# Kernel optimization log

Measured on AMD Instinct MI355X. Metric: run time of the kernel, lower is better.

## Reference

```python
import jax, jax.numpy as jnp
import numpy as np

D_MODEL = 1024
N_HEADS = 16
D_K = D_MODEL // N_HEADS
D_FF = 4096
B, S = 2, 2048
LN_EPS = 1e-5
NEG_INF = -1e30  # finite stand-in for -inf; first (all-masked) row is overwritten by zeros anyway


def layer_norm(x, g, b):
    mu = jnp.mean(x, axis=-1, keepdims=True)
    var = jnp.mean(jnp.square(x - mu), axis=-1, keepdims=True)
    return (x - mu) * jax.lax.rsqrt(var + LN_EPS) * g + b


def setup_inputs() -> dict:
    key = jax.random.key(0)
    ks = jax.random.split(key, 16)
    sd = 0.02
    inp = {
        "query": jax.random.normal(ks[0], (B, S, D_MODEL), jnp.float32),
        "key": jax.random.normal(ks[1], (B, S, D_MODEL), jnp.float32),
        "values": jax.random.normal(ks[2], (B, S, D_MODEL), jnp.float32),
        "Wq": jax.random.normal(ks[3], (D_MODEL, D_MODEL), jnp.float32) * sd,
        "bq": jnp.zeros((D_MODEL,), jnp.float32),
        "Wk": jax.random.normal(ks[4], (D_MODEL, D_MODEL), jnp.float32) * sd,
        "bk": jnp.zeros((D_MODEL,), jnp.float32),
        "Wv": jax.random.normal(ks[5], (D_MODEL, D_MODEL), jnp.float32) * sd,
        "bv": jnp.zeros((D_MODEL,), jnp.float32),
        "Wo": jax.random.normal(ks[6], (D_MODEL, D_MODEL), jnp.float32) * sd,
        "bo": jnp.zeros((D_MODEL,), jnp.float32),
        "ln1_g": jnp.ones((D_MODEL,), jnp.float32),
        "ln1_b": jnp.zeros((D_MODEL,), jnp.float32),
        "W1": jax.random.normal(ks[7], (D_MODEL, D_FF), jnp.float32) * sd,
        "b1": jnp.zeros((D_FF,), jnp.float32),
        "W2": jax.random.normal(ks[8], (D_FF, D_MODEL), jnp.float32) * sd,
        "b2": jnp.zeros((D_MODEL,), jnp.float32),
        "ln2_g": jnp.ones((D_MODEL,), jnp.float32),
        "ln2_b": jnp.zeros((D_MODEL,), jnp.float32),
        "mask": 0,
    }
    return inp


def reference(query, key, values, Wq, bq, Wk, bk, Wv, bv, Wo, bo,
              ln1_g, ln1_b, W1, b1, W2, b2, ln2_g, ln2_b, mask):
    b, s, d = query.shape
    # projections -> [B, H, S, d_k]
    q = (query @ Wq + bq).reshape(b, s, N_HEADS, D_K).transpose(0, 2, 1, 3)
    k = (key @ Wk + bk).reshape(b, s, N_HEADS, D_K).transpose(0, 2, 1, 3)
    v = (values @ Wv + bv).reshape(b, s, N_HEADS, D_K).transpose(0, 2, 1, 3)
    # scores [B, H, S, S]
    scores = jnp.einsum("bhqd,bhkd->bhqk", q, k) / jnp.sqrt(jnp.float32(D_K))
    # torch: triu(ones, k=mask)==0 -> allowed iff j < i + mask
    i = jnp.arange(s)[:, None]
    j = jnp.arange(s)[None, :]
    allowed = j < (i + mask)
    scores = jnp.where(allowed, scores, NEG_INF)
    attn = jax.nn.softmax(scores, axis=-1)
    if mask == 0:
        # zero-pad trick: first query row (fully masked) is replaced by zeros
        attn = attn.at[:, :, 0, :].set(0.0)
    ctx = jnp.einsum("bhqk,bhkd->bhqd", attn, v)
    ctx = ctx.transpose(0, 2, 1, 3).reshape(b, s, d)
    attn_out = ctx @ Wo + bo
    x = layer_norm(query + attn_out, ln1_g, ln1_b)
    ffn = jax.nn.relu(x @ W1 + b1) @ W2 + b2
    out = layer_norm(x + ffn, ln2_g, ln2_b)
    return out
```

## Files before the change

kernel.cpp:

```cpp
#include <hip/hip_runtime.h>


typedef __attribute__((ext_vector_type(8))) __bf16 bf16x8;
typedef __attribute__((ext_vector_type(4))) float f32x4;
typedef __attribute__((ext_vector_type(8))) short s16x8;

struct alignas(8)  S4 { short x, y, z, w; };
struct alignas(16) F4 { float x, y, z, w; };

static __device__ __forceinline__ short f2bf(float f) {
  unsigned u = __float_as_uint(f);
  u += 0x7fff + ((u >> 16) & 1);
  return (short)(u >> 16);
}

static __device__ __forceinline__ short f2bf_fast(float f) {
  union { __bf16 h; short s; } u;
  u.h = (__bf16)f;
  return u.s;
}

#if __has_builtin(__builtin_amdgcn_exp2f)
#define EXP2F(x) __builtin_amdgcn_exp2f(x)
#else
#define EXP2F(x) exp2f(x)
#endif
#define SM_SCALE 0.18033688011112042f

static __device__ __forceinline__ void store_out(float* p, float v) { *p = v; }
static __device__ __forceinline__ void store_out(short* p, float v) { *p = f2bf(v); }

#define GLL16(g, l)                                                         \
  __builtin_amdgcn_global_load_lds(                                         \
      (__attribute__((address_space(1))) void*)(g),                         \
      (__attribute__((address_space(3))) void*)(l), 16, 0, 0)

__global__ __launch_bounds__(256) void cvt_bf16_kernel(
    const float* __restrict__ i0, const float* __restrict__ i1,
    const float* __restrict__ i2, short* __restrict__ o0,
    short* __restrict__ o1, short* __restrict__ o2) {
  int z = blockIdx.y;
  const float* in = z == 0 ? i0 : (z == 1 ? i1 : i2);
  short* out = z == 0 ? o0 : (z == 1 ? o1 : o2);
  int i = (blockIdx.x * 256 + threadIdx.x) * 4;
  F4 v = *(const F4*)(in + i);
  S4 o = { f2bf(v.x), f2bf(v.y), f2bf(v.z), f2bf(v.w) };
  *(S4*)(out + i) = o;
}

__global__ __launch_bounds__(256) void transpose_cvt_kernel(
    const float* __restrict__ Wq, const float* __restrict__ Wk,
    const float* __restrict__ Wv, const float* __restrict__ Wo,
    const float* __restrict__ W1, const float* __restrict__ W2,
    short* __restrict__ Wqt, short* __restrict__ Wkt,
    short* __restrict__ Wvt, short* __restrict__ Wot,
    short* __restrict__ W1t, short* __restrict__ W2t) {
  __shared__ float tile[64][65];
  int bid = blockIdx.x;
  const float* W; short* Wt; int K, N, kx, ny;
  if (bid < 1024) {
    int w = bid >> 8, t = bid & 255;
    W = w == 0 ? Wq : (w == 1 ? Wk : (w == 2 ? Wv : Wo));
    Wt = w == 0 ? Wqt : (w == 1 ? Wkt : (w == 2 ? Wvt : Wot));
    K = 1024; N = 1024; kx = t & 15; ny = t >> 4;
  } else if (bid < 2048) {
    int t = bid - 1024;
    W = W1; Wt = W1t; K = 1024; N = 4096; kx = t & 15; ny = t >> 4;
  } else {
    int t = bid - 2048;
    W = W2; Wt = W2t; K = 4096; N = 1024; kx = t & 63; ny = t >> 6;
  }
  int k0 = kx * 64, n0 = ny * 64;
  int tid = threadIdx.x;
  int rr = tid >> 4, cc = (tid & 15) * 4;
#pragma unroll
  for (int p = 0; p < 4; ++p) {
    int row = p * 16 + rr;
    F4 v = *(const F4*)&W[(long)(k0 + row) * N + n0 + cc];
    tile[row][cc] = v.x; tile[row][cc + 1] = v.y;
    tile[row][cc + 2] = v.z; tile[row][cc + 3] = v.w;
  }
  __syncthreads();
#pragma unroll
  for (int p = 0; p < 4; ++p) {
    int rn = p * 16 + rr;
    S4 o = { f2bf(tile[cc + 0][rn]), f2bf(tile[cc + 1][rn]),
             f2bf(tile[cc + 2][rn]), f2bf(tile[cc + 3][rn]) };
    *(S4*)&Wt[(long)(n0 + rn) * K + k0 + cc] = o;
  }
}

template <int NF, int OUT_MODE, bool RELU, typename OT>
__device__ __forceinline__ void gemm256_core(
    const short* __restrict__ A, const short* __restrict__ Bt,
    const float* __restrict__ bias, OT* __restrict__ out,
    int N, int K, int kBeg, int kEnd, int m0, int n0) {
  constexpr int BN = NF * 64;
  constexpr int LB = BN / 64;
  __shared__ __align__(16) short sA[2][256 * 64];
  __shared__ __align__(16) short sB[2][BN * 64];
  int tid = threadIdx.x;
  int lane = tid & 63, wave = tid >> 6;
  int col = lane & 15, quad = lane >> 4;
  int wm = (wave >> 2) * 128;
  int wn = (wave & 3) * (NF * 16);

  f32x4 acc[8][NF] = {};

  const int NT = (kEnd - kBeg) >> 6;
  const int t0 = kBeg >> 6;

  auto stageA = [&](int buf, int kt) {
#pragma unroll
    for (int j = 0; j < 4; ++j) {
      int idx = j * 512 + tid;
      int row = idx >> 3, cp = idx & 7;
      int c = cp ^ (row & 7);
      GLL16(A + (long)(m0 + row) * K + kt * 64 + c * 8,
            &sA[buf][(j * 512 + (wave << 6)) * 8]);
    }
  };
  auto stageB = [&](int buf, int kt) {
#pragma unroll
    for (int j = 0; j < LB; ++j) {
      int idx = j * 512 + tid;
      int row = idx >> 3, cp = idx & 7;
      int c = cp ^ (row & 7);
      GLL16(Bt + (long)(n0 + row) * K + kt * 64 + c * 8,
            &sB[buf][(j * 512 + (wave << 6)) * 8]);
    }
  };

  stageA(0, t0);     stageB(0, t0);
  stageA(1, t0 + 1); stageB(1, t0 + 1);
  if constexpr (NF == 4) asm volatile("s_waitcnt vmcnt(8)" ::: "memory");
  else                   asm volatile("s_waitcnt vmcnt(6)" ::: "memory");
  __builtin_amdgcn_sched_barrier(0);
  __builtin_amdgcn_s_barrier();

  for (int t = 0; t < NT; ++t) {
    int cur = t & 1;
    bool pf = (t + 2 < NT);
    bf16x8 bf[NF][2], af[2][2];

#pragma unroll
    for (int n = 0; n < NF; ++n) {
      int rb = wn + n * 16 + col;
#pragma unroll
      for (int kk = 0; kk < 2; ++kk) {
        int ca = kk * 4 + quad;
        bf[n][kk] = *(const bf16x8*)&sB[cur][rb * 64 + ((ca ^ (rb & 7)) << 3)];
      }
    }
#pragma unroll
    for (int i = 0; i < 2; ++i) {
      int ra = wm + i * 16 + col;
#pragma unroll
      for (int kk = 0; kk < 2; ++kk) {
        int ca = kk * 4 + quad;
        af[i][kk] = *(const bf16x8*)&sA[cur][ra * 64 + ((ca ^ (ra & 7)) << 3)];
      }
    }
    asm volatile("s_waitcnt lgkmcnt(0)" ::: "memory");
    __builtin_amdgcn_sched_barrier(0);
    __builtin_amdgcn_s_setprio(1);
#pragma unroll
    for (int i = 0; i < 2; ++i)
#pragma unroll
      for (int n = 0; n < NF; ++n)
#pragma unroll
        for (int kk = 0; kk < 2; ++kk)
          acc[i][n] = __builtin_amdgcn_mfma_f32_16x16x32_bf16(
              af[i][kk], bf[n][kk], acc[i][n], 0, 0, 0);
    __builtin_amdgcn_s_setprio(0);
    __builtin_amdgcn_s_barrier();
    __builtin_amdgcn_sched_barrier(0);

    if (pf) stageB(cur, t0 + t + 2);
#pragma unroll
    for (int i = 0; i < 2; ++i) {
      int ra = wm + (2 + i) * 16 + col;
#pragma unroll
      for (int kk = 0; kk < 2; ++kk) {
        int ca = kk * 4 + quad;
        af[i][kk] = *(const bf16x8*)&sA[cur][ra * 64 + ((ca ^ (ra & 7)) << 3)];
      }
    }
    __builtin_amdgcn_s_setprio(1);
#pragma unroll
    for (int i = 0; i < 2; ++i)
#pragma unroll
      for (int n = 0; n < NF; ++n)
#pragma unroll
        for (int kk = 0; kk < 2; ++kk)
          acc[2 + i][n] = __builtin_amdgcn_mfma_f32_16x16x32_bf16(
              af[i][kk], bf[n][kk], acc[2 + i][n], 0, 0, 0);
    __builtin_amdgcn_s_setprio(0);
    __builtin_amdgcn_s_barrier();

#pragma unroll
    for (int i = 0; i < 2; ++i) {
      int ra = wm + (4 + i) * 16 + col;
#pragma unroll
      for (int kk = 0; kk < 2; ++kk) {
        int ca = kk * 4 + quad;
        af[i][kk] = *(const bf16x8*)&sA[cur][ra * 64 + ((ca ^ (ra & 7)) << 3)];
      }
    }
    __builtin_amdgcn_s_setprio(1);
#pragma unroll
    for (int i = 0; i < 2; ++i)
#pragma unroll
      for (int n = 0; n < NF; ++n)
#pragma unroll
        for (int kk = 0; kk < 2; ++kk)
          acc[4 + i][n] = __builtin_amdgcn_mfma_f32_16x16x32_bf16(
              af[i][kk], bf[n][kk], acc[4 + i][n], 0, 0, 0);
    __builtin_amdgcn_s_setprio(0);
    __builtin_amdgcn_s_barrier();

#pragma unroll
    for (int i = 0; i < 2; ++i) {
      int ra = wm + (6 + i) * 16 + col;
#pragma unroll
      for (int kk = 0; kk < 2; ++kk) {
        int ca = kk * 4 + quad;
        af[i][kk] = *(const bf16x8*)&sA[cur][ra * 64 + ((ca ^ (ra & 7)) << 3)];
      }
    }
    asm volatile("s_waitcnt lgkmcnt(0)" ::: "memory");
    __builtin_amdgcn_sched_barrier(0);
    __builtin_amdgcn_s_barrier();
    __builtin_amdgcn_sched_barrier(0);
    if (pf) stageA(cur, t0 + t + 2);
    __builtin_amdgcn_s_setprio(1);
#pragma unroll
    for (int i = 0; i < 2; ++i)
#pragma unroll
      for (int n = 0; n < NF; ++n)
#pragma unroll
        for (int kk = 0; kk < 2; ++kk)
          acc[6 + i][n] = __builtin_amdgcn_mfma_f32_16x16x32_bf16(
              af[i][kk], bf[n][kk], acc[6 + i][n], 0, 0, 0);
    __builtin_amdgcn_s_setprio(0);
    if (pf) {
      if constexpr (NF == 4) asm volatile("s_waitcnt vmcnt(8)" ::: "memory");
      else                   asm volatile("s_waitcnt vmcnt(6)" ::: "memory");
    } else {
      asm volatile("s_waitcnt vmcnt(0)" ::: "memory");
    }
    __builtin_amdgcn_sched_barrier(0);
    __builtin_amdgcn_s_barrier();
  }

#pragma unroll
  for (int m = 0; m < 8; ++m) {
#pragma unroll
    for (int n = 0; n < NF; ++n) {
      int Cc = n0 + wn + n * 16 + col;
      float bv = bias ? bias[Cc] : 0.f;
#pragma unroll
      for (int r = 0; r < 4; ++r) {
        int R = m0 + wm + m * 16 + quad * 4 + r;
        float v = acc[m][n][r] + bv;
        if (RELU) v = v > 0.f ? v : 0.f;
        if (OUT_MODE == 0) {
          store_out(&out[(long)R * N + Cc], v);
        } else {
          int bb = R >> 11, s = R & 2047, h = Cc >> 6, d = Cc & 63;
          store_out(&out[((long)((bb * 16 + h) * 2048 + s) << 6) + d], v);
        }
      }
    }
  }
}

__device__ __forceinline__ void gsp128_core(
    const short* __restrict__ A, const short* __restrict__ Bt,
    const float* __restrict__ bias, float* __restrict__ out,
    int N, int K, int kBeg, int kEnd, int m0, int n0) {
  __shared__ __align__(16) short sA[2][256 * 64];
  __shared__ __align__(16) short sB[2][128 * 64];
  int tid = threadIdx.x;
  int lane = tid & 63, wave = tid >> 6;
  int col = lane & 15, quad = lane >> 4;
  int wm = (wave >> 1) * 64;
  int wn = (wave & 1) * 64;

  f32x4 acc[4][4] = {};
  const int NT = (kEnd - kBeg) >> 6;
  const int t0 = kBeg >> 6;

  auto stageA = [&](int buf, int kt) {
#pragma unroll
    for (int j = 0; j < 4; ++j) {
      int idx = j * 512 + tid;
      int row = idx >> 3, cp = idx & 7;
      int c = cp ^ (row & 7);
      GLL16(A + (long)(m0 + row) * K + kt * 64 + c * 8,
            &sA[buf][(j * 512 + (wave << 6)) * 8]);
    }
  };
  auto stageB = [&](int buf, int kt) {
#pragma unroll
    for (int j = 0; j < 2; ++j) {
      int idx = j * 512 + tid;
      int row = idx >> 3, cp = idx & 7;
      int c = cp ^ (row & 7);
      GLL16(Bt + (long)(n0 + row) * K + kt * 64 + c * 8,
            &sB[buf][(j * 512 + (wave << 6)) * 8]);
    }
  };

  stageA(0, t0);     stageB(0, t0);
  stageA(1, t0 + 1); stageB(1, t0 + 1);
  asm volatile("s_waitcnt vmcnt(6)" ::: "memory");
  __builtin_amdgcn_s_barrier();

  for (int t = 0; t < NT; ++t) {
    int cur = t & 1;
    bool pf = (t + 2 < NT);
    bf16x8 bf[4][2], af[4][2];

#pragma unroll
    for (int n = 0; n < 4; ++n) {
      int rb = wn + n * 16 + col;
#pragma unroll
      for (int kk = 0; kk < 2; ++kk) {
        int ca = kk * 4 + quad;
        bf[n][kk] = *(const bf16x8*)&sB[cur][rb * 64 + ((ca ^ (rb & 7)) << 3)];
      }
    }
#pragma unroll
    for (int m = 0; m < 4; ++m) {
      int ra = wm + m * 16 + col;
#pragma unroll
      for (int kk = 0; kk < 2; ++kk) {
        int ca = kk * 4 + quad;
        af[m][kk] = *(const bf16x8*)&sA[cur][ra * 64 + ((ca ^ (ra & 7)) << 3)];
      }
    }
    asm volatile("s_waitcnt lgkmcnt(0)" ::: "memory");
    __builtin_amdgcn_s_barrier();
    __builtin_amdgcn_sched_barrier(0);
    if (pf) { stageA(cur, t0 + t + 2); stageB(cur, t0 + t + 2); }
    __builtin_amdgcn_s_setprio(1);
#pragma unroll
    for (int m = 0; m < 4; ++m)
#pragma unroll
      for (int n = 0; n < 4; ++n)
#pragma unroll
        for (int kk = 0; kk < 2; ++kk)
          acc[m][n] = __builtin_amdgcn_mfma_f32_16x16x32_bf16(
              af[m][kk], bf[n][kk], acc[m][n], 0, 0, 0);
    __builtin_amdgcn_s_setprio(0);
    if (pf) asm volatile("s_waitcnt vmcnt(6)" ::: "memory");
    else    asm volatile("s_waitcnt vmcnt(0)" ::: "memory");
    __builtin_amdgcn_s_barrier();
  }

#pragma unroll
  for (int m = 0; m < 4; ++m) {
#pragma unroll
    for (int n = 0; n < 4; ++n) {
      int Cc = n0 + wn + n * 16 + col;
      float bv = bias ? bias[Cc] : 0.f;
#pragma unroll
      for (int r = 0; r < 4; ++r) {
        int R = m0 + wm + m * 16 + quad * 4 + r;
        out[(long)R * N + Cc] = acc[m][n][r] + bv;
      }
    }
  }
}

__global__ __launch_bounds__(512) void g256_ffn1(
    const short* __restrict__ A, const short* __restrict__ Bt,
    const float* __restrict__ bias, short* __restrict__ out) {
  gemm256_core<4, 0, true, short>(A, Bt, bias, out, 4096, 1024, 0, 1024,
                                  blockIdx.x * 256, blockIdx.y * 256);
}

__global__ __launch_bounds__(512) void g256_qkv(
    const short* __restrict__ Aq, const short* __restrict__ Ak,
    const short* __restrict__ Av, const short* __restrict__ Btq,
    const short* __restrict__ Btk, const short* __restrict__ Btv,
    const float* __restrict__ bq, const float* __restrict__ bk,
    const float* __restrict__ bv, short* __restrict__ Qp,
    short* __restrict__ Kp, short* __restrict__ Vp) {
  int z = blockIdx.z;
  const short* A = z == 0 ? Aq : (z == 1 ? Ak : Av);
  const short* Bt = z == 0 ? Btq : (z == 1 ? Btk : Btv);
  const float* bias = z == 0 ? bq : (z == 1 ? bk : bv);
  short* out = z == 0 ? Qp : (z == 1 ? Kp : Vp);
  gemm256_core<4, 1, false, short>(A, Bt, bias, out, 1024, 1024, 0, 1024,
                                   blockIdx.x * 256, blockIdx.y * 256);
}

__global__ __launch_bounds__(512) void gsp_wo(
    const short* __restrict__ A, const short* __restrict__ Bt,
    const float* __restrict__ bias, float* __restrict__ p0,
    float* __restrict__ p1) {
  int z = blockIdx.z;
  float* out = z == 0 ? p0 : p1;
  const float* b = z == 0 ? bias : nullptr;
  gsp128_core(A, Bt, b, out, 1024, 1024, z * 512, z * 512 + 512,
              blockIdx.x * 256, blockIdx.y * 128);
}

__global__ __launch_bounds__(512) void gsp_ffn2(
    const short* __restrict__ A, const short* __restrict__ Bt,
    const float* __restrict__ bias, float* __restrict__ p0,
    float* __restrict__ p1) {
  int z = blockIdx.z;
  float* out = z == 0 ? p0 : p1;
  const float* b = z == 0 ? bias : nullptr;
  gsp128_core(A, Bt, b, out, 1024, 4096, z * 2048, z * 2048 + 2048,
              blockIdx.x * 256, blockIdx.y * 128);
}

__global__ __launch_bounds__(512) void attn_kernel(
    const short* __restrict__ Q, const short* __restrict__ K,
    const short* __restrict__ V, const int* __restrict__ maskp,
    short* __restrict__ ctx) {
  __shared__ __align__(16) short sK[2][64 * 64];
  __shared__ __align__(16) int   sVt[2][64 * 32];
  __shared__ __align__(16) short sP[8 * 32 * 64];
  __shared__ float sLred[128];
  int tid = threadIdx.x, wave = tid >> 6;
  int lane = tid & 63;
  int col = lane & 15, quad = lane >> 4;
  int g = wave >> 2, wlow = wave & 3;
  int bh = blockIdx.x, pair = blockIdx.y;
  int maskv = maskp[0];
  const long base = (long)bh * (2048 * 64);
  int b = bh >> 4, h = bh & 15;

  int kp = tid & 31, dg = tid >> 5, d0v = dg * 4;

  for (int pass = 0; pass < 2; ++pass) {
    int qt = pass ? (15 - pair) : pair;
    int iq0 = qt * 128 + wlow * 32;

    long jmax = (long)qt * 128 + 127 + maskv - 1;
    int tot = (jmax < 0) ? 0 : (int)(jmax >> 6) + 1;
    if (tot > 32) tot = 32;

    bf16x8 aQ[2][2];
#pragma unroll
    for (int mt = 0; mt < 2; ++mt)
#pragma unroll
      for (int kk = 0; kk < 2; ++kk)
        aQ[mt][kk] = *(const bf16x8*)&Q[base +
            (long)(iq0 + mt * 16 + col) * 64 + kk * 32 + quad * 8];

    f32x4 o[2][4] = {};
    float lsum[2][4] = {};

    if (tot > 0) {
      {
        int row = tid >> 3, cp = tid & 7;
        int c = cp ^ (row & 7);
        GLL16(K + base + (long)row * 64 + c * 8, &sK[0][(wave << 6) * 8]);
      }
      {
        union { S4 v; short s[4]; } u0, u1;
        u0.v = *(const S4*)&V[base + (long)(2 * kp) * 64 + d0v];
        u1.v = *(const S4*)&V[base + (long)(2 * kp + 1) * 64 + d0v];
#pragma unroll
        for (int j = 0; j < 4; ++j) {
          int d = d0v + j;
          int w = ((int)(unsigned short)u1.s[j] << 16) | (unsigned short)u0.s[j];
          sVt[0][d * 32 + ((((kp >> 2) ^ (d & 7)) << 2) | (kp & 3))] = w;
        }
      }
    }
    __syncthreads();

    for (int kt = 0; kt < tot; ++kt) {
      int cur = kt & 1, nxt = cur ^ 1;
      bool pf = (kt + 1 < tot);

      union { S4 v; short s[4]; } u0, u1;
      if (pf) {
        int row = tid >> 3, cp = tid & 7;
        int c = cp ^ (row & 7);
        GLL16(K + base + (long)((kt + 1) * 64 + row) * 64 + c * 8,
              &sK[nxt][(wave << 6) * 8]);
        u0.v = *(const S4*)&V[base + (long)((kt + 1) * 64 + 2 * kp) * 64 + d0v];
        u1.v = *(const S4*)&V[base + (long)((kt + 1) * 64 + 2 * kp + 1) * 64 + d0v];
      }

      f32x4 sc[2][2] = {};
      __builtin_amdgcn_s_setprio(1);
#pragma unroll
      for (int kk = 0; kk < 2; ++kk) {
        int ca = kk * 4 + quad;
#pragma unroll
        for (int nt = 0; nt < 2; ++nt) {
          int rk = (2 * g + nt) * 16 + col;
          bf16x8 bK = *(const bf16x8*)&sK[cur][rk * 64 + ((ca ^ (rk & 7)) << 3)];
#pragma unroll
          for (int mt = 0; mt < 2; ++mt)
            sc[mt][nt] = __builtin_amdgcn_mfma_f32_16x16x32_bf16(
                aQ[mt][kk], bK, sc[mt][nt], 0, 0, 0);
        }
      }
      __builtin_amdgcn_s_setprio(0);

      bool interior = (kt * 64 + g * 32 + 31) < (iq0 + maskv);
      if (interior) {
#pragma unroll
        for (int mt = 0; mt < 2; ++mt)
#pragma unroll
          for (int r = 0; r < 4; ++r) {
            int qr = mt * 16 + quad * 4 + r;
#pragma unroll
            for (int nt = 0; nt < 2; ++nt) {
              float p = EXP2F(sc[mt][nt][r] * SM_SCALE);
              lsum[mt][r] += p;
              int k8 = 4 * g + nt * 2 + (col >> 3);
              sP[wave * 2048 + qr * 64 + (((k8 ^ (qr & 7)) << 3) | (col & 7))] =
                  f2bf_fast(p);
            }
          }
      } else {
#pragma unroll
        for (int mt = 0; mt < 2; ++mt)
#pragma unroll
          for (int r = 0; r < 4; ++r) {
            int i = iq0 + mt * 16 + quad * 4 + r;
            int qr = mt * 16 + quad * 4 + r;
#pragma unroll
            for (int nt = 0; nt < 2; ++nt) {
              int j = kt * 64 + (2 * g + nt) * 16 + col;
              float p = (j < i + maskv) ? EXP2F(sc[mt][nt][r] * SM_SCALE) : 0.f;
              lsum[mt][r] += p;
              int k8 = 4 * g + nt * 2 + (col >> 3);
              sP[wave * 2048 + qr * 64 + (((k8 ^ (qr & 7)) << 3) | (col & 7))] =
                  f2bf_fast(p);
            }
          }
      }

      {
        int ca = 4 * g + quad;
        bf16x8 bV[4];
#pragma unroll
        for (int dt = 0; dt < 4; ++dt) {
          int d = dt * 16 + col;
          bV[dt] = *(const bf16x8*)((const short*)sVt[cur] + d * 64 +
                                    ((ca ^ (d & 7)) << 3));
        }
        __builtin_amdgcn_s_setprio(1);
#pragma unroll
        for (int mt = 0; mt < 2; ++mt) {
          int rp = mt * 16 + col;
          bf16x8 aP = *(const bf16x8*)&sP[wave * 2048 + rp * 64 +
                                          ((ca ^ (rp & 7)) << 3)];
#pragma unroll
          for (int dt = 0; dt < 4; ++dt)
            o[mt][dt] = __builtin_amdgcn_mfma_f32_16x16x32_bf16(
                aP, bV[dt], o[mt][dt], 0, 0, 0);
        }
        __builtin_amdgcn_s_setprio(0);
      }

      if (pf) {
#pragma unroll
        for (int j = 0; j < 4; ++j) {
          int d = d0v + j;
          int w = ((int)(unsigned short)u1.s[j] << 16) | (unsigned short)u0.s[j];
          sVt[nxt][d * 32 + ((((kp >> 2) ^ (d & 7)) << 2) | (kp & 3))] = w;
        }
      }
      __syncthreads();
    }

#pragma unroll
    for (int mt = 0; mt < 2; ++mt)
#pragma unroll
      for (int r = 0; r < 4; ++r)
#pragma unroll
        for (int off = 1; off < 16; off <<= 1)
          lsum[mt][r] += __shfl_xor(lsum[mt][r], off);

    float* od = (float*)sP;
    int slot = wlow * 64 + lane;
    if (g == 1) {
#pragma unroll
      for (int mt = 0; mt < 2; ++mt)
#pragma unroll
        for (int dt = 0; dt < 4; ++dt)
          *(f32x4*)&od[slot * 32 + (((mt * 4 + dt) ^ (lane & 7)) << 2)] =
              o[mt][dt];
      if (col == 0) {
#pragma unroll
        for (int mt = 0; mt < 2; ++mt)
#pragma unroll
          for (int r = 0; r < 4; ++r)
            sLred[wlow * 32 + mt * 16 + quad * 4 + r] = lsum[mt][r];
      }
    }
    __syncthreads();
    if (g == 0) {
#pragma unroll
      for (int mt = 0; mt < 2; ++mt) {
#pragma unroll
        for (int dt = 0; dt < 4; ++dt) {
          f32x4 t = *(const f32x4*)&od[slot * 32 +
                                       (((mt * 4 + dt) ^ (lane & 7)) << 2)];
          o[mt][dt] += t;
        }
      }
#pragma unroll
      for (int mt = 0; mt < 2; ++mt)
#pragma unroll
        for (int r = 0; r < 4; ++r) {
          float ls = lsum[mt][r] + sLred[wlow * 32 + mt * 16 + quad * 4 + r];
          int i = iq0 + mt * 16 + quad * 4 + r;
          float inv = (ls > 0.f) ? 1.f / ls : 0.f;
          if (maskv == 0 && i == 0) inv = 0.f;
#pragma unroll
          for (int dt = 0; dt < 4; ++dt)
            ctx[(long)(b * 2048 + i) * 1024 + h * 64 + dt * 16 + col] =
                f2bf(o[mt][dt][r] * inv);
        }
    }
    __syncthreads();
  }
}

__global__ __launch_bounds__(256) void ln_comb_kernel(
    const float* __restrict__ p0, const float* __restrict__ p1,
    const float* __restrict__ res, const float* __restrict__ g,
    const float* __restrict__ b, float* __restrict__ outf,
    short* __restrict__ outb) {
  int r = blockIdx.x, tid = threadIdx.x;
  int lane = tid & 63, wave = tid >> 6;
  long off0 = (long)r * 1024;
  F4 a = ((const F4*)(p0 + off0))[tid];
  F4 c = ((const F4*)(p1 + off0))[tid];
  F4 d = ((const F4*)(res + off0))[tid];
  F4 v = { a.x + c.x + d.x, a.y + c.y + d.y, a.z + c.z + d.z, a.w + c.w + d.w };
  float s = v.x + v.y + v.z + v.w;
  float sq = v.x * v.x + v.y * v.y + v.z * v.z + v.w * v.w;
#pragma unroll
  for (int off = 1; off < 64; off <<= 1) {
    s += __shfl_xor(s, off);
    sq += __shfl_xor(sq, off);
  }
  __shared__ float rs[4], rq[4];
  if (lane == 0) { rs[wave] = s; rq[wave] = sq; }
  __syncthreads();
  s = rs[0] + rs[1] + rs[2] + rs[3];
  sq = rq[0] + rq[1] + rq[2] + rq[3];
  float mu = s * (1.0f / 1024.0f);
  float var = sq * (1.0f / 1024.0f) - mu * mu;
  float rstd = rsqrtf(var + 1e-5f);
  F4 gv = ((const F4*)g)[tid], bv = ((const F4*)b)[tid];
  F4 o;
  o.x = (v.x - mu) * rstd * gv.x + bv.x;
  o.y = (v.y - mu) * rstd * gv.y + bv.y;
  o.z = (v.z - mu) * rstd * gv.z + bv.z;
  o.w = (v.w - mu) * rstd * gv.w + bv.w;
  ((F4*)(outf + off0))[tid] = o;
  if (outb) {
    S4 ob = { f2bf(o.x), f2bf(o.y), f2bf(o.z), f2bf(o.w) };
    ((S4*)(outb + off0))[tid] = ob;
  }
}

extern "C" void kernel_launch(void* const* d_in, const int* in_sizes, int n_in,
                              void* d_out, int out_size, void* d_ws, size_t ws_size,
                              hipStream_t stream) {
  const float* query  = (const float*)d_in[0];
  const float* keyi   = (const float*)d_in[1];
  const float* values = (const float*)d_in[2];
  const float* Wq = (const float*)d_in[3];
  const float* bq = (const float*)d_in[4];
  const float* Wk = (const float*)d_in[5];
  const float* bk = (const float*)d_in[6];
  const float* Wv = (const float*)d_in[7];
  const float* bv = (const float*)d_in[8];
  const float* Wo = (const float*)d_in[9];
  const float* bo = (const float*)d_in[10];
  const float* ln1_g = (const float*)d_in[11];
  const float* ln1_b = (const float*)d_in[12];
  const float* W1 = (const float*)d_in[13];
  const float* b1 = (const float*)d_in[14];
  const float* W2 = (const float*)d_in[15];
  const float* b2 = (const float*)d_in[16];
  const float* ln2_g = (const float*)d_in[17];
  const float* ln2_b = (const float*)d_in[18];
  const int*   maskp = (const int*)d_in[19];
  float* out = (float*)d_out;

  char* ws = (char*)d_ws;
  const size_t MB = 1u << 20;
  short* q_bf = (short*)(ws + 0);
  short* k_bf = (short*)(ws + 8 * MB);
  short* v_bf = (short*)(ws + 16 * MB);
  short* ctx  = (short*)(ws + 24 * MB);
  short* Qp   = (short*)(ws + 32 * MB);
  short* Kp   = (short*)(ws + 40 * MB);
  short* Vp   = (short*)(ws + 48 * MB);
  short* Wqt  = (short*)(ws + 56 * MB);
  short* Wkt  = (short*)(ws + 58 * MB);
  short* Wvt  = (short*)(ws + 60 * MB);
  short* Wot  = (short*)(ws + 62 * MB);
  short* W1t  = (short*)(ws + 64 * MB);
  short* W2t  = (short*)(ws + 72 * MB);
  short* hbuf = (short*)(ws + 80 * MB);
  float* pWo0 = (float*)(ws + 0);
  float* pWo1 = (float*)(ws + 32 * MB);
  float* x_f32 = (float*)(ws + 16 * MB);
  short* x_bf  = (short*)(ws + 48 * MB);
  float* pF0 = (float*)(ws + 0);
  float* pF1 = (float*)(ws + 32 * MB);

  cvt_bf16_kernel<<<dim3(4096, 3), 256, 0, stream>>>(query, keyi, values,
                                                     q_bf, k_bf, v_bf);
  transpose_cvt_kernel<<<3072, 256, 0, stream>>>(Wq, Wk, Wv, Wo, W1, W2,
                                                 Wqt, Wkt, Wvt, Wot, W1t, W2t);
  g256_qkv<<<dim3(16, 4, 3), 512, 0, stream>>>(q_bf, k_bf, v_bf,
                                               Wqt, Wkt, Wvt,
                                               bq, bk, bv, Qp, Kp, Vp);
  attn_kernel<<<dim3(32, 8), 512, 0, stream>>>(Qp, Kp, Vp, maskp, ctx);
  gsp_wo<<<dim3(16, 8, 2), 512, 0, stream>>>(ctx, Wot, bo, pWo0, pWo1);
  ln_comb_kernel<<<4096, 256, 0, stream>>>(pWo0, pWo1, query, ln1_g, ln1_b,
                                           x_f32, x_bf);
  g256_ffn1<<<dim3(16, 16), 512, 0, stream>>>(x_bf, W1t, b1, hbuf);
  gsp_ffn2<<<dim3(16, 8, 2), 512, 0, stream>>>(hbuf, W2t, b2, pF0, pF1);
  ln_comb_kernel<<<4096, 256, 0, stream>>>(pF0, pF1, x_f32, ln2_g, ln2_b,
                                           out, nullptr);

  (void)in_sizes; (void)n_in; (void)out_size; (void)ws_size;
}
```

Before: 382.7 us.

## Halve attention query tile to 64 rows with 256-thread blocks and more blocks

The attention kernel now processes 64-row query tiles per block with 4 waves (2 row groups by 2 key halves) instead of 128-row tiles with 8 waves. The grid doubles to 32x16, and causal pairing of tiles is adjusted to 31-pair. K/V staging loops are widened so each thread loads two K chunks and 8-wide V vectors, and the cross-group output reduction uses a simpler unswizzled layout. The intent is finer causal load balancing, more blocks across CUs and lower LDS per block, at the cost of loading K/V tiles once per 64 query rows instead of once per 128.

```diff
diff --git a/kernel.cpp b/kernel.cpp
--- a/kernel.cpp
+++ b/kernel.cpp
@@ -419,30 +419,30 @@
               blockIdx.x * 256, blockIdx.y * 128);
 }
 
-__global__ __launch_bounds__(512) void attn_kernel(
+__global__ __launch_bounds__(256) void attn_kernel(
     const short* __restrict__ Q, const short* __restrict__ K,
     const short* __restrict__ V, const int* __restrict__ maskp,
     short* __restrict__ ctx) {
   __shared__ __align__(16) short sK[2][64 * 64];
   __shared__ __align__(16) int   sVt[2][64 * 32];
-  __shared__ __align__(16) short sP[8 * 32 * 64];
-  __shared__ float sLred[128];
+  __shared__ __align__(16) short sP[4 * 32 * 64];
+  __shared__ float sLred[64];
   int tid = threadIdx.x, wave = tid >> 6;
   int lane = tid & 63;
   int col = lane & 15, quad = lane >> 4;
-  int g = wave >> 2, wlow = wave & 3;
+  int wlow = wave >> 1, g = wave & 1;
   int bh = blockIdx.x, pair = blockIdx.y;
   int maskv = maskp[0];
   const long base = (long)bh * (2048 * 64);
   int b = bh >> 4, h = bh & 15;
 
-  int kp = tid & 31, dg = tid >> 5, d0v = dg * 4;
+  int kp = tid & 31, dg = tid >> 5, d0v = dg * 8;
 
   for (int pass = 0; pass < 2; ++pass) {
-    int qt = pass ? (15 - pair) : pair;
-    int iq0 = qt * 128 + wlow * 32;
-
-    long jmax = (long)qt * 128 + 127 + maskv - 1;
+    int qt = pass ? (31 - pair) : pair;
+    int iq0 = qt * 64 + wlow * 32;
+
+    long jmax = (long)qt * 64 + 63 + maskv - 1;
     int tot = (jmax < 0) ? 0 : (int)(jmax >> 6) + 1;
     if (tot > 32) tot = 32;
 
@@ -458,19 +458,21 @@
     float lsum[2][4] = {};
 
     if (tot > 0) {
+#pragma unroll
+      for (int j = 0; j < 2; ++j) {
+        int idx = j * 256 + tid;
+        int row = idx >> 3, cp = idx & 7;
+        int c = cp ^ (row & 7);
+        GLL16(K + base + (long)row * 64 + c * 8,
+              &sK[0][(j * 256 + (wave << 6)) * 8]);
+      }
       {
-        int row = tid >> 3, cp = tid & 7;
-        int c = cp ^ (row & 7);
-        GLL16(K + base + (long)row * 64 + c * 8, &sK[0][(wave << 6) * 8]);
-      }
-      {
-        union { S4 v; short s[4]; } u0, u1;
-        u0.v = *(const S4*)&V[base + (long)(2 * kp) * 64 + d0v];
-        u1.v = *(const S4*)&V[base + (long)(2 * kp + 1) * 64 + d0v];
-#pragma unroll
-        for (int j = 0; j < 4; ++j) {
+        s16x8 u0 = *(const s16x8*)&V[base + (long)(2 * kp) * 64 + d0v];
+        s16x8 u1 = *(const s16x8*)&V[base + (long)(2 * kp + 1) * 64 + d0v];
+#pragma unroll
+        for (int j = 0; j < 8; ++j) {
           int d = d0v + j;
-          int w = ((int)(unsigned short)u1.s[j] << 16) | (unsigned short)u0.s[j];
+          int w = ((int)(unsigned short)u1[j] << 16) | (unsigned short)u0[j];
           sVt[0][d * 32 + ((((kp >> 2) ^ (d & 7)) << 2) | (kp & 3))] = w;
         }
       }
@@ -481,14 +483,18 @@
       int cur = kt & 1, nxt = cur ^ 1;
       bool pf = (kt + 1 < tot);
 
-      union { S4 v; short s[4]; } u0, u1;
+      s16x8 u0, u1;
       if (pf) {
-        int row = tid >> 3, cp = tid & 7;
-        int c = cp ^ (row & 7);
-        GLL16(K + base + (long)((kt + 1) * 64 + row) * 64 + c * 8,
-              &sK[nxt][(wave << 6) * 8]);
-        u0.v = *(const S4*)&V[base + (long)((kt + 1) * 64 + 2 * kp) * 64 + d0v];
-        u1.v = *(const S4*)&V[base + (long)((kt + 1) * 64 + 2 * kp + 1) * 64 + d0v];
+#pragma unroll
+        for (int j = 0; j < 2; ++j) {
+          int idx = j * 256 + tid;
+          int row = idx >> 3, cp = idx & 7;
+          int c = cp ^ (row & 7);
+          GLL16(K + base + (long)((kt + 1) * 64 + row) * 64 + c * 8,
+                &sK[nxt][(j * 256 + (wave << 6)) * 8]);
+        }
+        u0 = *(const s16x8*)&V[base + (long)((kt + 1) * 64 + 2 * kp) * 64 + d0v];
+        u1 = *(const s16x8*)&V[base + (long)((kt + 1) * 64 + 2 * kp + 1) * 64 + d0v];
       }
 
       f32x4 sc[2][2] = {};
@@ -568,9 +574,9 @@
 
       if (pf) {
 #pragma unroll
-        for (int j = 0; j < 4; ++j) {
+        for (int j = 0; j < 8; ++j) {
           int d = d0v + j;
-          int w = ((int)(unsigned short)u1.s[j] << 16) | (unsigned short)u0.s[j];
+          int w = ((int)(unsigned short)u1[j] << 16) | (unsigned short)u0[j];
           sVt[nxt][d * 32 + ((((kp >> 2) ^ (d & 7)) << 2) | (kp & 3))] = w;
         }
       }
@@ -585,15 +591,14 @@
         for (int off = 1; off < 16; off <<= 1)
           lsum[mt][r] += __shfl_xor(lsum[mt][r], off);
 
-    float* od = (float*)sP;
+    f32x4* odv = (f32x4*)sP;
     int slot = wlow * 64 + lane;
     if (g == 1) {
 #pragma unroll
       for (int mt = 0; mt < 2; ++mt)
 #pragma unroll
         for (int dt = 0; dt < 4; ++dt)
-          *(f32x4*)&od[slot * 32 + (((mt * 4 + dt) ^ (lane & 7)) << 2)] =
-              o[mt][dt];
+          odv[(mt * 4 + dt) * 128 + slot] = o[mt][dt];
       if (col == 0) {
 #pragma unroll
         for (int mt = 0; mt < 2; ++mt)
@@ -605,14 +610,10 @@
     __syncthreads();
     if (g == 0) {
 #pragma unroll
-      for (int mt = 0; mt < 2; ++mt) {
-#pragma unroll
-        for (int dt = 0; dt < 4; ++dt) {
-          f32x4 t = *(const f32x4*)&od[slot * 32 +
-                                       (((mt * 4 + dt) ^ (lane & 7)) << 2)];
-          o[mt][dt] += t;
-        }
-      }
+      for (int mt = 0; mt < 2; ++mt)
+#pragma unroll
+        for (int dt = 0; dt < 4; ++dt)
+          o[mt][dt] += odv[(mt * 4 + dt) * 128 + slot];
 #pragma unroll
       for (int mt = 0; mt < 2; ++mt)
 #pragma unroll
@@ -726,7 +727,7 @@
   g256_qkv<<<dim3(16, 4, 3), 512, 0, stream>>>(q_bf, k_bf, v_bf,
                                                Wqt, Wkt, Wvt,
                                                bq, bk, bv, Qp, Kp, Vp);
-  attn_kernel<<<dim3(32, 8), 512, 0, stream>>>(Qp, Kp, Vp, maskp, ctx);
+  attn_kernel<<<dim3(32, 16), 256, 0, stream>>>(Qp, Kp, Vp, maskp, ctx);
   gsp_wo<<<dim3(16, 8, 2), 512, 0, stream>>>(ctx, Wot, bo, pWo0, pWo1);
   ln_comb_kernel<<<4096, 256, 0, stream>>>(pWo0, pWo1, query, ln1_g, ln1_b,
                                            x_f32, x_bf);
```

Measured after the change: 371.1 us. -3.0%, faster.
